# Kernel optimization log

Measured on AMD Instinct MI355X. Metric: run time of the kernel, lower is better.

The kernel has to match this reference:

```python
import jax, jax.numpy as jnp
import numpy as np

N = 40000      # nodes
E = 320000     # edges (avg degree 8)
F = 512        # feats_in_size
H = 256        # num_hidden_nodes
HEADS = 8      # num_attention_heads
NEG_SLOPE = 0.01  # torch LeakyReLU default


def setup_inputs() -> dict:
    key = jax.random.key(0)
    k = jax.random.split(key, 8)
    feats = jax.random.normal(k[0], (N, F), jnp.float32)
    # strictly upper-triangular edges (dst > src) so the original module's
    # in-place sequential update equals the parallel segment-softmax GAT
    src = jax.random.randint(k[1], (E,), 0, N - 1, dtype=jnp.int32)
    dst = src + jax.random.randint(k[2], (E,), 1, N - src, dtype=jnp.int32)
    adj_ind = jnp.stack([src, dst], axis=0)  # [2, E]
    adjacency_matrix = jnp.zeros((1, 1), jnp.float32)  # unused when adj_ind given
    W_w = jax.random.normal(k[3], (F, H), jnp.float32) * 0.05   # Linear weight (transposed)
    W_b = jax.random.normal(k[4], (H,), jnp.float32) * 0.05
    attn_w = jax.random.normal(k[5], (HEADS, 2 * H), jnp.float32) * 0.05  # per-head [1,2H] stacked
    attn_b = jax.random.normal(k[6], (HEADS,), jnp.float32) * 0.05
    return {"feats": feats, "adjacency_matrix": adjacency_matrix, "adj_ind": adj_ind,
            "W_w": W_w, "W_b": W_b, "attn_w": attn_w, "attn_b": attn_b}


def reference(feats, adjacency_matrix, adj_ind, W_w, W_b, attn_w, attn_b):
    src, dst = adj_ind[0], adj_ind[1]
    h = feats @ W_w + W_b                       # [N, H]
    h_src = h[src]                              # [E, H] gather
    h_dst = h[dst]                              # [E, H] gather
    # attn_i(cat(h_src, h_dst)) == h_src @ a_i[:H] + h_dst @ a_i[H:] + b_i
    a_s, a_d = attn_w[:, :H], attn_w[:, H:]     # [HEADS, H] each
    scores = h_src @ a_s.T + h_dst @ a_d.T + attn_b  # [E, HEADS]
    scores = jax.nn.leaky_relu(scores, NEG_SLOPE)
    # segment softmax over outgoing edges of each src node
    m = jax.ops.segment_max(scores, src, num_segments=N)   # [N, HEADS]
    ex = jnp.exp(scores - m[src])
    denom = jax.ops.segment_sum(ex, src, num_segments=N)   # [N, HEADS]
    alpha = ex / denom[src]                                 # [E, HEADS]
    # per-head: out_i[u] = h[u] + sum_{(u,v)} alpha_i(u,v) * h[v]
    outs = [h + jax.ops.segment_sum(alpha[:, i:i + 1] * h_dst, src, num_segments=N)
            for i in range(HEADS)]
    return jnp.concatenate(outs, axis=1)        # [N, HEADS*H]
```

## Files before the change

### kernel.cpp

```cpp
#include <hip/hip_runtime.h>

typedef __attribute__((ext_vector_type(8))) short short8v;
typedef __attribute__((ext_vector_type(4))) float f32x4;

#define NN 40000
#define FF 512
#define HH 256
#define EE 320000
#define NHEADS 8
#define NEG_SLOPE 0.01f
#define NB 157

__device__ __forceinline__ short f2bf(float x) {
    unsigned u = __float_as_uint(x);
    u += 0x7fffu + ((u >> 16) & 1u);
    return (short)(u >> 16);
}
__device__ __forceinline__ float bf2f(unsigned short b) {
    return __uint_as_float(((unsigned)b) << 16);
}

__global__ void prep_kernel(const float* __restrict__ W, short* __restrict__ Wt,
                            int* __restrict__ p) {
    int b = blockIdx.x;
    if (b < 512) {
        int i = b * 256 + threadIdx.x;
        int k = i >> 8, n = i & 255;
        Wt[n * 512 + k] = f2bf(W[i]);
    } else {
        int i = (b - 512) * 256 + threadIdx.x;
        if (i < 2 * NN) p[i] = 0;
    }
}

__global__ __launch_bounds__(512) void gemm_kernel(
    const float* __restrict__ feats,
    const short* __restrict__ Btf,
    const float* __restrict__ bias,
    unsigned short* __restrict__ h2)
{
    __shared__ short8v ldsA[512];
    __shared__ short8v ldsB[2048];
    const int tid = threadIdx.x;
    const int lane = tid & 63, w = tid >> 6;
    const int wm = w >> 2, wn = w & 3;
    const int r0 = blockIdx.x * 64;

    const int arow = tid >> 3, aslot = tid & 7;

    float4 regA[2];
    short8v regB[4];

    auto stage_loadA = [&](int k0) {
        const float* p = feats + (size_t)(r0 + arow) * 512 + k0 + aslot * 8;
        regA[0] = *reinterpret_cast<const float4*>(p);
        regA[1] = *reinterpret_cast<const float4*>(p + 4);
    };
    auto stage_loadB = [&](int k0) {
        #pragma unroll
        for (int c = 0; c < 4; ++c) {
            int u = tid + c * 512;
            int row = u >> 3, slot = u & 7;
            regB[c] = *reinterpret_cast<const short8v*>(Btf + (size_t)row * 512 + k0 + slot * 8);
        }
    };
    auto stage_store = [&]() {
        short8v v;
        #pragma unroll
        for (int j = 0; j < 4; ++j) {
            v[j]     = f2bf(regA[0][j]);
            v[4 + j] = f2bf(regA[1][j]);
        }
        ldsA[arow * 8 + (aslot ^ (arow & 7))] = v;
        #pragma unroll
        for (int c = 0; c < 4; ++c) {
            int u = tid + c * 512;
            int row = u >> 3, slot = u & 7;
            ldsB[row * 8 + (slot ^ (row & 7))] = regB[c];
        }
    };

    f32x4 acc[2][4];
    #pragma unroll
    for (int i = 0; i < 2; ++i)
        #pragma unroll
        for (int j = 0; j < 4; ++j)
            acc[i][j] = {0.f, 0.f, 0.f, 0.f};

    stage_loadA(0);
    stage_loadB(0);

    for (int kt = 0; kt < 8; ++kt) {
        __syncthreads();
        stage_store();
        __syncthreads();
        if (kt < 7) {
            stage_loadA((kt + 1) * 64);
            stage_loadB((kt + 1) * 64);
        }
        #pragma unroll
        for (int kc = 0; kc < 2; ++kc) {
            short8v af[2], bfr[4];
            int kslot = kc * 4 + (lane >> 4);
            #pragma unroll
            for (int mr = 0; mr < 2; ++mr) {
                int row = wm * 32 + mr * 16 + (lane & 15);
                af[mr] = ldsA[row * 8 + (kslot ^ (row & 7))];
            }
            #pragma unroll
            for (int nr = 0; nr < 4; ++nr) {
                int col = wn * 64 + nr * 16 + (lane & 15);
                bfr[nr] = ldsB[col * 8 + (kslot ^ (col & 7))];
            }
            #pragma unroll
            for (int mr = 0; mr < 2; ++mr)
                #pragma unroll
                for (int nr = 0; nr < 4; ++nr)
                    acc[mr][nr] = __builtin_amdgcn_mfma_f32_16x16x32_bf16(
                        af[mr], bfr[nr], acc[mr][nr], 0, 0, 0);
        }
    }

    #pragma unroll
    for (int mr = 0; mr < 2; ++mr) {
        #pragma unroll
        for (int nr = 0; nr < 4; ++nr) {
            int gc = wn * 64 + nr * 16 + (lane & 15);
            float b = bias[gc];
            #pragma unroll
            for (int j = 0; j < 4; ++j) {
                int gr = r0 + wm * 32 + mr * 16 + (lane >> 4) * 4 + j;
                h2[(size_t)gr * 256 + gc] = (unsigned short)f2bf(acc[mr][nr][j] + b);
            }
        }
    }
}

__global__ __launch_bounds__(256) void sproj_kernel(
    const unsigned short* __restrict__ h2, const float* __restrict__ attn_w,
    float* __restrict__ s_src, float* __restrict__ s_dst)
{
    int wid = threadIdx.x >> 6, lane = threadIdx.x & 63;
    int n = blockIdx.x * 4 + wid;
    if (n >= NN) return;
    ushort4 hb = *reinterpret_cast<const ushort4*>(h2 + (size_t)n * 256 + lane * 4);
    float4 hv = {bf2f(hb.x), bf2f(hb.y), bf2f(hb.z), bf2f(hb.w)};

    float ss[8], sd[8];
    #pragma unroll
    for (int q = 0; q < 8; ++q) {
        float4 as = *reinterpret_cast<const float4*>(attn_w + q * 512 + lane * 4);
        float4 ad = *reinterpret_cast<const float4*>(attn_w + q * 512 + 256 + lane * 4);
        ss[q] = hv.x * as.x + hv.y * as.y + hv.z * as.z + hv.w * as.w;
        sd[q] = hv.x * ad.x + hv.y * ad.y + hv.z * ad.z + hv.w * ad.w;
    }
    #pragma unroll
    for (int q = 0; q < 8; ++q) {
        #pragma unroll
        for (int off = 32; off >= 1; off >>= 1) {
            ss[q] += __shfl_xor(ss[q], off);
            sd[q] += __shfl_xor(sd[q], off);
        }
    }
    if (lane == 0) {
        #pragma unroll
        for (int q = 0; q < 8; ++q) {
            s_src[(size_t)n * 8 + q] = ss[q];
            s_dst[(size_t)n * 8 + q] = sd[q];
        }
    }
}

__global__ void edge_kernel(const int* __restrict__ src, const int* __restrict__ dst,
                            const float* __restrict__ s_src, const float* __restrict__ s_dst,
                            const float* __restrict__ attn_b,
                            float* __restrict__ escores, int* __restrict__ deg)
{
    int e = blockIdx.x * 256 + threadIdx.x;
    if (e >= EE) return;
    int s = src[e], d = dst[e];
    float4 a0 = reinterpret_cast<const float4*>(s_src + (size_t)s * 8)[0];
    float4 a1 = reinterpret_cast<const float4*>(s_src + (size_t)s * 8)[1];
    float4 c0 = reinterpret_cast<const float4*>(s_dst + (size_t)d * 8)[0];
    float4 c1 = reinterpret_cast<const float4*>(s_dst + (size_t)d * 8)[1];
    float4 b0 = reinterpret_cast<const float4*>(attn_b)[0];
    float4 b1 = reinterpret_cast<const float4*>(attn_b)[1];
    float v[8];
    v[0] = a0.x + c0.x + b0.x; v[1] = a0.y + c0.y + b0.y;
    v[2] = a0.z + c0.z + b0.z; v[3] = a0.w + c0.w + b0.w;
    v[4] = a1.x + c1.x + b1.x; v[5] = a1.y + c1.y + b1.y;
    v[6] = a1.z + c1.z + b1.z; v[7] = a1.w + c1.w + b1.w;
    #pragma unroll
    for (int q = 0; q < 8; ++q) {
        float sc = v[q] > 0.f ? v[q] : NEG_SLOPE * v[q];
        v[q] = __expf(sc);
    }
    float4 o0 = {v[0], v[1], v[2], v[3]};
    float4 o1 = {v[4], v[5], v[6], v[7]};
    reinterpret_cast<float4*>(escores + (size_t)e * 8)[0] = o0;
    reinterpret_cast<float4*>(escores + (size_t)e * 8)[1] = o1;
    atomicAdd(&deg[s], 1);
}

__global__ __launch_bounds__(256) void scan1_kernel(const int* __restrict__ deg,
                                                    int* __restrict__ rowtmp,
                                                    int* __restrict__ partials)
{
    __shared__ int buf[256];
    int tid = threadIdx.x;
    int i = blockIdx.x * 256 + tid;
    int v = (i < NN) ? deg[i] : 0;
    buf[tid] = v;
    __syncthreads();
    #pragma unroll
    for (int off = 1; off < 256; off <<= 1) {
        int t = (tid >= off) ? buf[tid - off] : 0;
        __syncthreads();
        buf[tid] += t;
        __syncthreads();
    }
    if (i < NN) rowtmp[i] = buf[tid] - v;
    if (tid == 255) partials[blockIdx.x] = buf[255];
}

__global__ __launch_bounds__(256) void scan23_kernel(const int* __restrict__ rowtmp,
                                                     const int* __restrict__ partials,
                                                     int* __restrict__ rowstart)
{
    __shared__ int buf[256];
    __shared__ int offs[256];
    int tid = threadIdx.x;
    int v = (tid < NB) ? partials[tid] : 0;
    buf[tid] = v;
    __syncthreads();
    #pragma unroll
    for (int off = 1; off < 256; off <<= 1) {
        int t = (tid >= off) ? buf[tid - off] : 0;
        __syncthreads();
        buf[tid] += t;
        __syncthreads();
    }
    offs[tid] = buf[tid] - v;
    __syncthreads();
    int myoff = offs[blockIdx.x];
    int i = blockIdx.x * 256 + tid;
    if (i < NN) rowstart[i] = rowtmp[i] + myoff;
    if (blockIdx.x == 0 && tid == 0) rowstart[NN] = EE;
}

__global__ void fill_kernel(const int* __restrict__ src, const int* __restrict__ dst,
                            const int* __restrict__ rowstart,
                            int* __restrict__ cursor, int2* __restrict__ csrPack)
{
    int e = blockIdx.x * 256 + threadIdx.x;
    if (e >= EE) return;
    int s = src[e];
    int pos = atomicAdd(&cursor[s], 1);
    csrPack[rowstart[s] + pos] = make_int2(e, dst[e]);
}

__global__ __launch_bounds__(256) void agg_kernel(
    const unsigned short* __restrict__ h2,
    const float* __restrict__ escores,
    const int2* __restrict__ csrPack, const int* __restrict__ rowstart,
    float* __restrict__ out)
{
    int wid = threadIdx.x >> 6, lane = threadIdx.x & 63;
    int n = blockIdx.x * 4 + wid;
    if (n >= NN) return;
    int start = rowstart[n];
    int deg = rowstart[n + 1] - start;
    int ei = lane >> 3, hh = lane & 7;

    ushort4 sb = *reinterpret_cast<const ushort4*>(h2 + (size_t)n * 256 + lane * 4);
    f32x4 hv = {bf2f(sb.x), bf2f(sb.y), bf2f(sb.z), bf2f(sb.w)};
    f32x4 acc[8];
    #pragma unroll
    for (int q = 0; q < 8; ++q) acc[q] = {0.f, 0.f, 0.f, 0.f};
    float den = 0.f;

    for (int base = 0; base < deg; base += 8) {
        int idx = base + ei;
        int dd = 0; float ex = 0.f;
        if (idx < deg) {
            int2 p = csrPack[start + idx];
            dd = p.y;
            ex = escores[(size_t)p.x * 8 + hh];
        }
        den += ex;
        int cnt = min(8, deg - base);
        for (int t = 0; t < cnt; ++t) {
            int ddt = __shfl(dd, t * 8);
            ushort4 hb = *reinterpret_cast<const ushort4*>(h2 + (size_t)ddt * 256 + lane * 4);
            f32x4 hd = {bf2f(hb.x), bf2f(hb.y), bf2f(hb.z), bf2f(hb.w)};
            #pragma unroll
            for (int q = 0; q < 8; ++q) {
                float exq = __shfl(ex, t * 8 + q);
                acc[q] += hd * exq;
            }
        }
    }

    den += __shfl_xor(den, 8);
    den += __shfl_xor(den, 16);
    den += __shfl_xor(den, 32);

    float* orow = out + (size_t)n * 2048;
    #pragma unroll
    for (int q = 0; q < 8; ++q) {
        float dq = __shfl(den, q);
        float r = dq > 0.f ? 1.f / dq : 0.f;
        f32x4 o = hv + acc[q] * r;
        *reinterpret_cast<f32x4*>(orow + q * 256 + lane * 4) = o;
    }
}

extern "C" void kernel_launch(void* const* d_in, const int* in_sizes, int n_in,
                              void* d_out, int out_size, void* d_ws, size_t ws_size,
                              hipStream_t stream) {
    const float* feats  = (const float*)d_in[0];
    const int*   adj    = (const int*)d_in[2];
    const float* W_w    = (const float*)d_in[3];
    const float* W_b    = (const float*)d_in[4];
    const float* attn_w = (const float*)d_in[5];
    const float* attn_b = (const float*)d_in[6];
    float* out = (float*)d_out;
    const int* srcA = adj;
    const int* dstA = adj + EE;

    char* ws = (char*)d_ws;
    size_t off = 0;
    auto alloc = [&](size_t bytes) -> void* {
        void* p = ws + off;
        off += (bytes + 255) & ~(size_t)255;
        return p;
    };
    short* Wt            = (short*)alloc((size_t)HH * FF * 2);
    unsigned short* h2   = (unsigned short*)alloc((size_t)NN * HH * 2);
    float* s_src   = (float*)alloc((size_t)NN * 8 * 4);
    float* s_dst   = (float*)alloc((size_t)NN * 8 * 4);
    float* escores = (float*)alloc((size_t)EE * 8 * 4);
    int*   deg     = (int*)alloc((size_t)NN * 4 * 2);
    int*   cursor  = deg + NN;
    int*   rowtmp  = (int*)alloc((size_t)NN * 4);
    int*   partials= (int*)alloc((size_t)256 * 4);
    int*   rowstart= (int*)alloc((size_t)(NN + 1) * 4);
    int2*  csrPack = (int2*)alloc((size_t)EE * 8);

    prep_kernel<<<512 + (2 * NN + 255) / 256, 256, 0, stream>>>(W_w, Wt, deg);
    gemm_kernel<<<NN / 64, 512, 0, stream>>>(feats, Wt, W_b, h2);
    sproj_kernel<<<NN / 4, 256, 0, stream>>>(h2, attn_w, s_src, s_dst);
    edge_kernel<<<(EE + 255) / 256, 256, 0, stream>>>(srcA, dstA, s_src, s_dst, attn_b, escores, deg);
    scan1_kernel<<<NB, 256, 0, stream>>>(deg, rowtmp, partials);
    scan23_kernel<<<NB, 256, 0, stream>>>(rowtmp, partials, rowstart);
    fill_kernel<<<(EE + 255) / 256, 256, 0, stream>>>(srcA, dstA, rowstart, cursor, csrPack);
    agg_kernel<<<NN / 4, 256, 0, stream>>>(h2, escores, csrPack, rowstart, out);
}
```

Before: 217.3 us.

## Fuse edge scoring with CSR fill and store exp scores in CSR order

Degree counting moves into the prep kernel, so the prefix scan runs before the GEMM. The edge kernel then computes the exp scores and writes them straight into CSR slot order along with the dst index. This removes the separate fill kernel and the indirect escores gather in aggregation, which now reads its scores contiguously per node. In exchange it adds a memset and more atomics in prep, and the scattered 32-byte score writes are uncoalesced.

```diff
diff --git a/kernel.cpp b/kernel.cpp
--- a/kernel.cpp
+++ b/kernel.cpp
@@ -21,15 +21,15 @@
 }
 
 __global__ void prep_kernel(const float* __restrict__ W, short* __restrict__ Wt,
-                            int* __restrict__ p) {
+                            const int* __restrict__ src, int* __restrict__ deg) {
     int b = blockIdx.x;
     if (b < 512) {
         int i = b * 256 + threadIdx.x;
         int k = i >> 8, n = i & 255;
         Wt[n * 512 + k] = f2bf(W[i]);
     } else {
-        int i = (b - 512) * 256 + threadIdx.x;
-        if (i < 2 * NN) p[i] = 0;
+        int e = (b - 512) * 256 + threadIdx.x;
+        if (e < EE) atomicAdd(&deg[src[e]], 1);
     }
 }
 
@@ -171,10 +171,57 @@
     }
 }
 
-__global__ void edge_kernel(const int* __restrict__ src, const int* __restrict__ dst,
-                            const float* __restrict__ s_src, const float* __restrict__ s_dst,
-                            const float* __restrict__ attn_b,
-                            float* __restrict__ escores, int* __restrict__ deg)
+__global__ __launch_bounds__(256) void scan1_kernel(const int* __restrict__ deg,
+                                                    int* __restrict__ rowtmp,
+                                                    int* __restrict__ partials)
+{
+    __shared__ int buf[256];
+    int tid = threadIdx.x;
+    int i = blockIdx.x * 256 + tid;
+    int v = (i < NN) ? deg[i] : 0;
+    buf[tid] = v;
+    __syncthreads();
+    #pragma unroll
+    for (int off = 1; off < 256; off <<= 1) {
+        int t = (tid >= off) ? buf[tid - off] : 0;
+        __syncthreads();
+        buf[tid] += t;
+        __syncthreads();
+    }
+    if (i < NN) rowtmp[i] = buf[tid] - v;
+    if (tid == 255) partials[blockIdx.x] = buf[255];
+}
+
+__global__ __launch_bounds__(256) void scan23_kernel(const int* __restrict__ rowtmp,
+                                                     const int* __restrict__ partials,
+                                                     int* __restrict__ rowstart)
+{
+    __shared__ int buf[256];
+    __shared__ int offs[256];
+    int tid = threadIdx.x;
+    int v = (tid < NB) ? partials[tid] : 0;
+    buf[tid] = v;
+    __syncthreads();
+    #pragma unroll
+    for (int off = 1; off < 256; off <<= 1) {
+        int t = (tid >= off) ? buf[tid - off] : 0;
+        __syncthreads();
+        buf[tid] += t;
+        __syncthreads();
+    }
+    offs[tid] = buf[tid] - v;
+    __syncthreads();
+    int myoff = offs[blockIdx.x];
+    int i = blockIdx.x * 256 + tid;
+    if (i < NN) rowstart[i] = rowtmp[i] + myoff;
+    if (blockIdx.x == 0 && tid == 0) rowstart[NN] = EE;
+}
+
+__global__ void edgefill_kernel(const int* __restrict__ src, const int* __restrict__ dst,
+                                const float* __restrict__ s_src, const float* __restrict__ s_dst,
+                                const float* __restrict__ attn_b,
+                                const int* __restrict__ rowstart, int* __restrict__ cursor,
+                                int* __restrict__ csrDst, float* __restrict__ exSlot)
 {
     int e = blockIdx.x * 256 + threadIdx.x;
     if (e >= EE) return;
@@ -195,74 +242,19 @@
         float sc = v[q] > 0.f ? v[q] : NEG_SLOPE * v[q];
         v[q] = __expf(sc);
     }
+    int pos = atomicAdd(&cursor[s], 1);
+    int slot = rowstart[s] + pos;
+    csrDst[slot] = d;
     float4 o0 = {v[0], v[1], v[2], v[3]};
     float4 o1 = {v[4], v[5], v[6], v[7]};
-    reinterpret_cast<float4*>(escores + (size_t)e * 8)[0] = o0;
-    reinterpret_cast<float4*>(escores + (size_t)e * 8)[1] = o1;
-    atomicAdd(&deg[s], 1);
-}
-
-__global__ __launch_bounds__(256) void scan1_kernel(const int* __restrict__ deg,
-                                                    int* __restrict__ rowtmp,
-                                                    int* __restrict__ partials)
-{
-    __shared__ int buf[256];
-    int tid = threadIdx.x;
-    int i = blockIdx.x * 256 + tid;
-    int v = (i < NN) ? deg[i] : 0;
-    buf[tid] = v;
-    __syncthreads();
-    #pragma unroll
-    for (int off = 1; off < 256; off <<= 1) {
-        int t = (tid >= off) ? buf[tid - off] : 0;
-        __syncthreads();
-        buf[tid] += t;
-        __syncthreads();
-    }
-    if (i < NN) rowtmp[i] = buf[tid] - v;
-    if (tid == 255) partials[blockIdx.x] = buf[255];
-}
-
-__global__ __launch_bounds__(256) void scan23_kernel(const int* __restrict__ rowtmp,
-                                                     const int* __restrict__ partials,
-                                                     int* __restrict__ rowstart)
-{
-    __shared__ int buf[256];
-    __shared__ int offs[256];
-    int tid = threadIdx.x;
-    int v = (tid < NB) ? partials[tid] : 0;
-    buf[tid] = v;
-    __syncthreads();
-    #pragma unroll
-    for (int off = 1; off < 256; off <<= 1) {
-        int t = (tid >= off) ? buf[tid - off] : 0;
-        __syncthreads();
-        buf[tid] += t;
-        __syncthreads();
-    }
-    offs[tid] = buf[tid] - v;
-    __syncthreads();
-    int myoff = offs[blockIdx.x];
-    int i = blockIdx.x * 256 + tid;
-    if (i < NN) rowstart[i] = rowtmp[i] + myoff;
-    if (blockIdx.x == 0 && tid == 0) rowstart[NN] = EE;
-}
-
-__global__ void fill_kernel(const int* __restrict__ src, const int* __restrict__ dst,
-                            const int* __restrict__ rowstart,
-                            int* __restrict__ cursor, int2* __restrict__ csrPack)
-{
-    int e = blockIdx.x * 256 + threadIdx.x;
-    if (e >= EE) return;
-    int s = src[e];
-    int pos = atomicAdd(&cursor[s], 1);
-    csrPack[rowstart[s] + pos] = make_int2(e, dst[e]);
+    reinterpret_cast<float4*>(exSlot + (size_t)slot * 8)[0] = o0;
+    reinterpret_cast<float4*>(exSlot + (size_t)slot * 8)[1] = o1;
 }
 
 __global__ __launch_bounds__(256) void agg_kernel(
     const unsigned short* __restrict__ h2,
-    const float* __restrict__ escores,
-    const int2* __restrict__ csrPack, const int* __restrict__ rowstart,
+    const float* __restrict__ exSlot,
+    const int* __restrict__ csrDst, const int* __restrict__ rowstart,
     float* __restrict__ out)
 {
     int wid = threadIdx.x >> 6, lane = threadIdx.x & 63;
@@ -270,7 +262,7 @@
     if (n >= NN) return;
     int start = rowstart[n];
     int deg = rowstart[n + 1] - start;
-    int ei = lane >> 3, hh = lane & 7;
+    int ei = lane >> 3;
 
     ushort4 sb = *reinterpret_cast<const ushort4*>(h2 + (size_t)n * 256 + lane * 4);
     f32x4 hv = {bf2f(sb.x), bf2f(sb.y), bf2f(sb.z), bf2f(sb.w)};
@@ -281,12 +273,11 @@
 
     for (int base = 0; base < deg; base += 8) {
         int idx = base + ei;
-        int dd = 0; float ex = 0.f;
-        if (idx < deg) {
-            int2 p = csrPack[start + idx];
-            dd = p.y;
-            ex = escores[(size_t)p.x * 8 + hh];
-        }
+        int dd = 0;
+        if (idx < deg) dd = csrDst[start + idx];
+        float ex = 0.f;
+        int lpos = base * 8 + lane;
+        if (lpos < deg * 8) ex = exSlot[(size_t)start * 8 + lpos];
         den += ex;
         int cnt = min(8, deg - base);
         for (int t = 0; t < cnt; ++t) {
@@ -339,20 +330,21 @@
     unsigned short* h2   = (unsigned short*)alloc((size_t)NN * HH * 2);
     float* s_src   = (float*)alloc((size_t)NN * 8 * 4);
     float* s_dst   = (float*)alloc((size_t)NN * 8 * 4);
-    float* escores = (float*)alloc((size_t)EE * 8 * 4);
+    float* exSlot  = (float*)alloc((size_t)EE * 8 * 4);
     int*   deg     = (int*)alloc((size_t)NN * 4 * 2);
     int*   cursor  = deg + NN;
     int*   rowtmp  = (int*)alloc((size_t)NN * 4);
     int*   partials= (int*)alloc((size_t)256 * 4);
     int*   rowstart= (int*)alloc((size_t)(NN + 1) * 4);
-    int2*  csrPack = (int2*)alloc((size_t)EE * 8);
-
-    prep_kernel<<<512 + (2 * NN + 255) / 256, 256, 0, stream>>>(W_w, Wt, deg);
+    int*   csrDst  = (int*)alloc((size_t)EE * 4);
+
+    hipMemsetAsync(deg, 0, (size_t)2 * NN * 4, stream);
+    prep_kernel<<<512 + (EE + 255) / 256, 256, 0, stream>>>(W_w, Wt, srcA, deg);
+    scan1_kernel<<<NB, 256, 0, stream>>>(deg, rowtmp, partials);
+    scan23_kernel<<<NB, 256, 0, stream>>>(rowtmp, partials, rowstart);
     gemm_kernel<<<NN / 64, 512, 0, stream>>>(feats, Wt, W_b, h2);
     sproj_kernel<<<NN / 4, 256, 0, stream>>>(h2, attn_w, s_src, s_dst);
-    edge_kernel<<<(EE + 255) / 256, 256, 0, stream>>>(srcA, dstA, s_src, s_dst, attn_b, escores, deg);
-    scan1_kernel<<<NB, 256, 0, stream>>>(deg, rowtmp, partials);
-    scan23_kernel<<<NB, 256, 0, stream>>>(rowtmp, partials, rowstart);
-    fill_kernel<<<(EE + 255) / 256, 256, 0, stream>>>(srcA, dstA, rowstart, cursor, csrPack);
-    agg_kernel<<<NN / 4, 256, 0, stream>>>(h2, escores, csrPack, rowstart, out);
-}
+    edgefill_kernel<<<(EE + 255) / 256, 256, 0, stream>>>(srcA, dstA, s_src, s_dst, attn_b,
+                                                          rowstart, cursor, csrDst, exSlot);
+    agg_kernel<<<NN / 4, 256, 0, stream>>>(h2, exSlot, csrDst, rowstart, out);
+}
```

Measured after the change: 214.5 us. Within noise of the previous version (-1.3%).
